# Performance work log

Hardware: AMD Instinct MI355X
Metric: run time of the kernel (lower is better)

Reference implementation:

```python
import jax, jax.numpy as jnp
import numpy as np

NUM_NEIGHBORS = 9  # init kwarg num_neighbors


def euclidean_dist(x, y):
    # Pairwise L2 distance, matching PatchcoreModel.euclidean_dist
    x_norm = jnp.sum(x * x, axis=-1, keepdims=True)
    y_norm = jnp.sum(y * y, axis=-1, keepdims=True)
    res = x_norm - 2.0 * jnp.matmul(x, jnp.swapaxes(y, -2, -1)) + jnp.swapaxes(y_norm, -2, -1)
    return jnp.sqrt(jnp.maximum(res, 0.0))


def setup_inputs() -> dict:
    key = jax.random.key(0)
    k1, k2 = jax.random.split(key)
    B, W, H, D, M = 8, 28, 28, 384, 32768
    embedding = jax.random.normal(k1, (B * W * H, D), dtype=jnp.float32)
    memory_bank = jax.random.normal(k2, (M, D), dtype=jnp.float32)
    return {"embedding": embedding, "memory_bank": memory_bank,
            "batch_size": B, "width": W, "height": H}


def reference(embedding, memory_bank, batch_size, width, height):
    # nearest_neighbors(embedding, n_neighbors=1)
    d = euclidean_dist(embedding, memory_bank)          # [N, M]
    patch_scores = jnp.min(d, axis=1)                   # [N]
    locations = jnp.argmin(d, axis=1)                   # [N]

    ps = patch_scores.reshape(batch_size, -1)           # [B, P]
    loc = locations.reshape(batch_size, -1)             # [B, P]

    # compute_anomaly_score (num_neighbors > 1 path)
    bidx = jnp.arange(batch_size)
    max_patches = jnp.argmax(ps, axis=1)                # [B]
    emb_b = embedding.reshape(batch_size, -1, embedding.shape[-1])
    max_feats = emb_b[bidx, max_patches]                # [B, D]
    score = ps[bidx, max_patches]                       # [B]
    nn_index = loc[bidx, max_patches]                   # [B]
    nn_sample = memory_bank[nn_index]                   # [B, D]

    k = min(NUM_NEIGHBORS, memory_bank.shape[0])
    d2 = euclidean_dist(nn_sample, memory_bank)         # [B, M]
    _, support = jax.lax.top_k(-d2, k)                  # k smallest, ascending

    d3 = euclidean_dist(max_feats[:, None, :], memory_bank[support])  # [B, 1, k]
    weights = (1.0 - jax.nn.softmax(d3[:, 0, :], axis=1))[:, 0]       # [B]
    pred_score = weights * score                        # [B]

    patch_map = ps.reshape(batch_size, 1, width, height)
    return patch_map, pred_score
```

## Files before the change

kernel.cpp:

```cpp
#include <hip/hip_runtime.h>
#include <hip/hip_bf16.h>

#define NROWS 6272
#define MROWS 32768
#define DDIM  384
#define NB    8
#define PPB   784
#define BN    128
#define BMT   128
#define MSPLIT 16
#define MC    (MROWS / MSPLIT)
#define MTILES (MC / BMT)
#define NSTEPS (MTILES * 12)
#define PSW   (MSPLIT * 2)
#define KNN   9
#define TSEG  16
#define TOPT  3
#define NRESC (NB * TOPT)

typedef float f32x4 __attribute__((ext_vector_type(4)));
typedef short bf16x8 __attribute__((ext_vector_type(8)));

__device__ __forceinline__ unsigned short f2bf(float f) {
  union { float f; unsigned int u; } c; c.f = f;
  unsigned int u = c.u + 0x7FFFu + ((c.u >> 16) & 1u);
  return (unsigned short)(u >> 16);
}
__device__ __forceinline__ unsigned int pk2(float a, float b) {
  return (unsigned int)f2bf(a) | ((unsigned int)f2bf(b) << 16);
}
__device__ __forceinline__ float wredsum(float v) {
#pragma unroll
  for (int m = 32; m; m >>= 1) v += __shfl_xor(v, m, 64);
  return v;
}
__device__ __forceinline__ void glds16(const void* g, void* l) {
  __builtin_amdgcn_global_load_lds(
      (const __attribute__((address_space(1))) unsigned int*)g,
      (__attribute__((address_space(3))) unsigned int*)l, 16, 0, 0);
}

__global__ __launch_bounds__(256) void cvt_bf16_kernel(
    const float* __restrict__ src, unsigned short* __restrict__ dst) {
  const int i = blockIdx.x * 256 + threadIdx.x;
  const float4 a = ((const float4*)src)[i * 2];
  const float4 b = ((const float4*)src)[i * 2 + 1];
  uint4 o = { pk2(a.x, a.y), pk2(a.z, a.w), pk2(b.x, b.y), pk2(b.z, b.w) };
  ((uint4*)dst)[i] = o;
}

__global__ __launch_bounds__(256) void rownorm_kernel(
    const float* __restrict__ src, float* __restrict__ nrm) {
  const int wave = threadIdx.x >> 6, lane = threadIdx.x & 63;
  const int m = blockIdx.x * 4 + wave;
  const float* y = src + (size_t)m * DDIM;
  float s = 0.f;
#pragma unroll
  for (int j = 0; j < 6; ++j) { float v = y[lane + 64 * j]; s = fmaf(v, v, s); }
  s = wredsum(s);
  if (lane == 0) nrm[m] = s;
}

__global__ __launch_bounds__(256) void dist_min_kernel(
    const unsigned short* __restrict__ embbf, const unsigned short* __restrict__ bankbf,
    const float* __restrict__ ynorm, float* __restrict__ psPart) {
  __shared__ unsigned short Al[2][4096];
  __shared__ unsigned short Bl[2][4096];
  __shared__ float ynLds[MC];

  const int bid = blockIdx.x;
  const int ms = bid & (MSPLIT - 1);
  const int bn = bid >> 4;
  const int t = threadIdx.x;
  const int lane = t & 63;
  const int wave = t >> 6;
  const int wn = wave >> 1, wm = wave & 1;
  const int l15 = lane & 15, l4 = lane >> 4;

  for (int i = t; i < MC; i += 256) ynLds[i] = ynorm[ms * MC + i];

  const int seg0 = wave * 2, seg1 = seg0 + 1;
  const int sRow = lane >> 2;
  const int sColB = (lane & 3) * 16;
  const char* aG0 = (const char*)embbf + ((size_t)(bn * BN + seg0 * 16 + sRow)) * 768 + sColB;
  const char* aG1 = (const char*)embbf + ((size_t)(bn * BN + seg1 * 16 + sRow)) * 768 + sColB;
  const char* bG0 = (const char*)bankbf + ((size_t)(ms * MC + seg0 * 16 + sRow)) * 768 + sColB;
  const char* bG1 = (const char*)bankbf + ((size_t)(ms * MC + seg1 * 16 + sRow)) * 768 + sColB;

  auto stage = [&](int st, int buf) {
    const int kb = (st % 12) * 64;
    const size_t bOff = (size_t)(st / 12) * (BMT * 768);
    glds16(aG0 + kb, &Al[buf][seg0 * 512]);
    glds16(aG1 + kb, &Al[buf][seg1 * 512]);
    glds16(bG0 + bOff + kb, &Bl[buf][seg0 * 512]);
    glds16(bG1 + bOff + kb, &Bl[buf][seg1 * 512]);
  };

  f32x4 acc[4][4];
#pragma unroll
  for (int nf = 0; nf < 4; ++nf)
#pragma unroll
    for (int mf = 0; mf < 4; ++mf) {
      acc[nf][mf][0] = 0.f; acc[nf][mf][1] = 0.f;
      acc[nf][mf][2] = 0.f; acc[nf][mf][3] = 0.f;
    }
  float rm[4][4];
#pragma unroll
  for (int a = 0; a < 4; ++a)
#pragma unroll
    for (int b = 0; b < 4; ++b) rm[a][b] = 3.4e38f;

  stage(0, 0);
  __syncthreads();

  for (int st = 0; st < NSTEPS; ++st) {
    const int buf = st & 1;
    if (st < NSTEPS - 1) stage(st + 1, buf ^ 1);

    bf16x8 af[4], bfr[4];
#pragma unroll
    for (int nf = 0; nf < 4; ++nf)
      af[nf] = *(const bf16x8*)&Al[buf][(wn * 64 + nf * 16 + l15) * 32 + l4 * 8];
#pragma unroll
    for (int mf = 0; mf < 4; ++mf)
      bfr[mf] = *(const bf16x8*)&Bl[buf][(wm * 64 + mf * 16 + l15) * 32 + l4 * 8];
#pragma unroll
    for (int nf = 0; nf < 4; ++nf)
#pragma unroll
      for (int mf = 0; mf < 4; ++mf)
        acc[nf][mf] = __builtin_amdgcn_mfma_f32_16x16x32_bf16(
            af[nf], bfr[mf], acc[nf][mf], 0, 0, 0);

    if ((st % 12) == 11) {
      const int mt = st / 12;
      const int mb = mt * BMT + wm * 64 + l15;
#pragma unroll
      for (int mf = 0; mf < 4; ++mf) {
        const float yv = ynLds[mb + mf * 16];
#pragma unroll
        for (int nf = 0; nf < 4; ++nf)
#pragma unroll
          for (int r = 0; r < 4; ++r)
            rm[nf][r] = fminf(rm[nf][r], fmaf(-2.f, acc[nf][mf][r], yv));
      }
#pragma unroll
      for (int nf = 0; nf < 4; ++nf)
#pragma unroll
        for (int mf = 0; mf < 4; ++mf) {
          acc[nf][mf][0] = 0.f; acc[nf][mf][1] = 0.f;
          acc[nf][mf][2] = 0.f; acc[nf][mf][3] = 0.f;
        }
    }
    __syncthreads();
  }

#pragma unroll
  for (int nf = 0; nf < 4; ++nf)
#pragma unroll
    for (int r = 0; r < 4; ++r) {
      float v = rm[nf][r];
      v = fminf(v, __shfl_xor(v, 1, 64));
      v = fminf(v, __shfl_xor(v, 2, 64));
      v = fminf(v, __shfl_xor(v, 4, 64));
      v = fminf(v, __shfl_xor(v, 8, 64));
      if (l15 == 0) {
        const int n = bn * BN + wn * 64 + nf * 16 + l4 * 4 + r;
        psPart[(size_t)n * PSW + ms * 2 + wm] = v;
      }
    }
}

__global__ __launch_bounds__(256) void ps_reduce_kernel(
    const float* __restrict__ psPart, const float* __restrict__ xnorm,
    float* __restrict__ out) {
  const int n = blockIdx.x * 256 + threadIdx.x;
  if (n >= NROWS) return;
  const float4* p = (const float4*)(psPart + (size_t)n * PSW);
  float m = 3.4e38f;
#pragma unroll
  for (int j = 0; j < 8; ++j) {
    const float4 a = p[j];
    m = fminf(m, fminf(fminf(a.x, a.y), fminf(a.z, a.w)));
  }
  out[n] = sqrtf(fmaxf(xnorm[n] + m, 0.f));
}

__global__ __launch_bounds__(256) void argmax3_kernel(
    const float* __restrict__ ps, int* __restrict__ trow) {
  __shared__ float vals[PPB];
  __shared__ float sv[256]; __shared__ int si[256];
  const int b = blockIdx.x, t = threadIdx.x;
  for (int p = t; p < PPB; p += 256) vals[p] = ps[b * PPB + p];
  __syncthreads();
  for (int k = 0; k < TOPT; ++k) {
    float best = -3.4e38f; int bi = 0x7FFFFFFF;
    for (int p = t; p < PPB; p += 256) {
      const float v = vals[p];
      if (v > best || (v == best && p < bi)) { best = v; bi = p; }
    }
    sv[t] = best; si[t] = bi;
    __syncthreads();
    for (int s = 128; s > 0; s >>= 1) {
      if (t < s) {
        if (sv[t + s] > sv[t] || (sv[t + s] == sv[t] && si[t + s] < si[t])) {
          sv[t] = sv[t + s]; si[t] = si[t + s];
        }
      }
      __syncthreads();
    }
    if (t == 0) { trow[b * TOPT + k] = b * PPB + si[0]; vals[si[0]] = -3.4e38f; }
    __syncthreads();
  }
}

__global__ __launch_bounds__(256) void rescue_kernel(
    const float* __restrict__ emb, const float* __restrict__ bank,
    const float* __restrict__ ynorm, const int* __restrict__ trow,
    float* __restrict__ rscV, int* __restrict__ rscI) {
  __shared__ float xs[NRESC][DDIM];
  __shared__ int sTrow[NRESC];
  __shared__ float pvw[4][NRESC]; __shared__ int piw[4][NRESC];
  const int t = threadIdx.x, lane = t & 63, wave = t >> 6;
  if (t < NRESC) sTrow[t] = trow[t];
  __syncthreads();
  for (int j = 0; j < NRESC; ++j)
    for (int k = t; k < DDIM; k += 256) xs[j][k] = emb[(size_t)sTrow[j] * DDIM + k];
  __syncthreads();

  const int m = blockIdx.x * 256 + t;
  const float yn = ynorm[m];
  const float* y = bank + (size_t)m * DDIM;
  float accs[NRESC];
#pragma unroll
  for (int j = 0; j < NRESC; ++j) accs[j] = yn;
  for (int k = 0; k < DDIM; ++k) {
    const float bk2 = -2.f * y[k];
#pragma unroll
    for (int j = 0; j < NRESC; ++j) accs[j] = fmaf(bk2, xs[j][k], accs[j]);
  }
#pragma unroll
  for (int j = 0; j < NRESC; ++j) {
    float v = accs[j]; int mi = m;
#pragma unroll
    for (int s = 1; s < 64; s <<= 1) {
      const float ov = __shfl_xor(v, s, 64);
      const int oi = __shfl_xor(mi, s, 64);
      if (ov < v || (ov == v && oi < mi)) { v = ov; mi = oi; }
    }
    if (lane == 0) { pvw[wave][j] = v; piw[wave][j] = mi; }
  }
  __syncthreads();
  if (t < NRESC) {
    float bv = pvw[0][t]; int bi = piw[0][t];
#pragma unroll
    for (int w = 1; w < 4; ++w)
      if (pvw[w][t] < bv || (pvw[w][t] == bv && piw[w][t] < bi)) { bv = pvw[w][t]; bi = piw[w][t]; }
    rscV[(size_t)t * 128 + blockIdx.x] = bv;
    rscI[(size_t)t * 128 + blockIdx.x] = bi;
  }
}

__global__ __launch_bounds__(256) void rescue_merge_kernel(
    const float* __restrict__ emb, const int* __restrict__ trow,
    const float* __restrict__ rscV, const int* __restrict__ rscI,
    float* __restrict__ score, int* __restrict__ maxrow, int* __restrict__ nnidx) {
  __shared__ float xnLds[NRESC];
  __shared__ float exv[NRESC]; __shared__ int exi[NRESC];
  const int t = threadIdx.x, lane = t & 63, wave = t >> 6;
  for (int q = 0; q < 6; ++q) {
    const int j = wave * 6 + q;
    const float* x = emb + (size_t)trow[j] * DDIM;
    float s = 0.f;
#pragma unroll
    for (int e = 0; e < 6; ++e) { const float v = x[lane + 64 * e]; s = fmaf(v, v, s); }
    s = wredsum(s);
    if (lane == 0) xnLds[j] = s;
  }
  __syncthreads();
  if (t < NRESC) {
    float bv = 3.4e38f; int bi = 0x7FFFFFFF;
    for (int i = 0; i < 128; ++i) {
      const float v = rscV[(size_t)t * 128 + i];
      if (v < bv) { bv = v; bi = rscI[(size_t)t * 128 + i]; }
      else if (v == bv) { const int oi = rscI[(size_t)t * 128 + i]; if (oi < bi) bi = oi; }
    }
    exv[t] = sqrtf(fmaxf(xnLds[t] + bv, 0.f));
    exi[t] = bi;
  }
  __syncthreads();
  if (t < NB) {
    float best = -3.4e38f; int bj = 0, brow = 0x7FFFFFFF;
    for (int k = 0; k < TOPT; ++k) {
      const int j = t * TOPT + k;
      const int row = trow[j];
      if (exv[j] > best || (exv[j] == best && row < brow)) { best = exv[j]; bj = j; brow = row; }
    }
    score[t] = best; maxrow[t] = brow; nnidx[t] = exi[bj];
  }
}

__global__ __launch_bounds__(256) void d2_kernel(
    const float* __restrict__ bank, const float* __restrict__ ynorm,
    const int* __restrict__ nnidx, float* __restrict__ d2) {
  __shared__ float nnf[NB][DDIM];
  __shared__ float nno[NB];
  const int t = threadIdx.x;
  for (int b = 0; b < NB; ++b) {
    const int m = nnidx[b];
    for (int j = t; j < DDIM; j += 256) nnf[b][j] = bank[(size_t)m * DDIM + j];
  }
  if (t < NB) nno[t] = ynorm[nnidx[t]];
  __syncthreads();
  const int wave = t >> 6, lane = t & 63;
  const int m = blockIdx.x * 4 + wave;
  const float* y = bank + (size_t)m * DDIM;
  float yv[6];
#pragma unroll
  for (int j = 0; j < 6; ++j) yv[j] = y[lane + 64 * j];
  const float yn = ynorm[m];
  for (int b = 0; b < NB; ++b) {
    float d = 0.f;
#pragma unroll
    for (int j = 0; j < 6; ++j) d = fmaf(yv[j], nnf[b][lane + 64 * j], d);
    d = wredsum(d);
    if (lane == 0) d2[(size_t)b * MROWS + m] = fmaxf(fmaf(-2.f, d, nno[b] + yn), 0.f);
  }
}

__global__ __launch_bounds__(256) void topk1_kernel(
    const float* __restrict__ d2, float* __restrict__ tv, int* __restrict__ ti) {
  __shared__ float sv[256]; __shared__ int si[256];
  const int b = blockIdx.x / TSEG, seg = blockIdx.x % TSEG;
  const float* base = d2 + (size_t)b * MROWS + seg * 2048;
  const int t = threadIdx.x, off = t * 8;
  float v[8];
  const float4 x0 = *(const float4*)(base + off);
  const float4 x1 = *(const float4*)(base + off + 4);
  v[0] = x0.x; v[1] = x0.y; v[2] = x0.z; v[3] = x0.w;
  v[4] = x1.x; v[5] = x1.y; v[6] = x1.z; v[7] = x1.w;
  for (int k = 0; k < KNN; ++k) {
    float lb = v[0]; int li = 0;
#pragma unroll
    for (int i = 1; i < 8; ++i)
      if (v[i] < lb) { lb = v[i]; li = i; }
    sv[t] = lb; si[t] = off + li;
    __syncthreads();
    for (int s = 128; s > 0; s >>= 1) {
      if (t < s) {
        if (sv[t + s] < sv[t] || (sv[t + s] == sv[t] && si[t + s] < si[t])) {
          sv[t] = sv[t + s]; si[t] = si[t + s];
        }
      }
      __syncthreads();
    }
    const int widx = si[0];
    if (t == 0) {
      tv[(size_t)(b * TSEG + seg) * KNN + k] = sv[0];
      ti[(size_t)(b * TSEG + seg) * KNN + k] = seg * 2048 + widx;
    }
    __syncthreads();
#pragma unroll
    for (int i = 0; i < 8; ++i)
      if (off + i == widx) v[i] = 3.4e38f;
  }
}

__global__ __launch_bounds__(64) void topk2_kernel(
    const float* __restrict__ tv, const int* __restrict__ ti, int* __restrict__ support) {
  const int b = blockIdx.x, lane = threadIdx.x;
  float v[3]; int ix[3];
#pragma unroll
  for (int j = 0; j < 3; ++j) {
    const int e = lane + j * 64;
    if (e < TSEG * KNN) { v[j] = tv[(size_t)b * TSEG * KNN + e]; ix[j] = ti[(size_t)b * TSEG * KNN + e]; }
    else { v[j] = 3.4e38f; ix[j] = 0x7FFFFFFF; }
  }
  for (int k = 0; k < KNN; ++k) {
    float bv = v[0]; int bi = ix[0];
#pragma unroll
    for (int j = 1; j < 3; ++j)
      if (v[j] < bv || (v[j] == bv && ix[j] < bi)) { bv = v[j]; bi = ix[j]; }
#pragma unroll
    for (int m = 1; m < 64; m <<= 1) {
      const float ov = __shfl_xor(bv, m, 64);
      const int oi = __shfl_xor(bi, m, 64);
      if (ov < bv || (ov == bv && oi < bi)) { bv = ov; bi = oi; }
    }
    if (lane == 0) support[b * KNN + k] = bi;
#pragma unroll
    for (int j = 0; j < 3; ++j)
      if (ix[j] == bi) v[j] = 3.4e38f;
  }
}

__global__ __launch_bounds__(256) void final_kernel(
    const float* __restrict__ emb, const float* __restrict__ bank,
    const float* __restrict__ ynorm, const int* __restrict__ support,
    const int* __restrict__ maxrow, const float* __restrict__ score,
    float* __restrict__ pred) {
  __shared__ float d3s[NB][KNN];
  const int t = threadIdx.x, wave = t >> 6, lane = t & 63;
  for (int b = wave; b < NB; b += 4) {
    const float* x = emb + (size_t)maxrow[b] * DDIM;
    float xv[6];
#pragma unroll
    for (int j = 0; j < 6; ++j) xv[j] = x[lane + 64 * j];
    float xn = 0.f;
#pragma unroll
    for (int j = 0; j < 6; ++j) xn = fmaf(xv[j], xv[j], xn);
    xn = wredsum(xn);
    for (int k = 0; k < KNN; ++k) {
      const int m = support[b * KNN + k];
      const float* y = bank + (size_t)m * DDIM;
      float d = 0.f;
#pragma unroll
      for (int j = 0; j < 6; ++j) d = fmaf(xv[j], y[lane + 64 * j], d);
      d = wredsum(d);
      if (lane == 0) d3s[b][k] = sqrtf(fmaxf(fmaf(-2.f, d, xn + ynorm[m]), 0.f));
    }
  }
  __syncthreads();
  if (t < NB) {
    float mx = -3.4e38f;
    for (int k = 0; k < KNN; ++k) mx = fmaxf(mx, d3s[t][k]);
    float sum = 0.f, e0 = 0.f;
    for (int k = 0; k < KNN; ++k) {
      const float e = expf(d3s[t][k] - mx);
      if (k == 0) e0 = e;
      sum += e;
    }
    pred[t] = (1.f - e0 / sum) * score[t];
  }
}

extern "C" void kernel_launch(void* const* d_in, const int* in_sizes, int n_in,
                              void* d_out, int out_size, void* d_ws, size_t ws_size,
                              hipStream_t stream) {
  (void)in_sizes; (void)n_in; (void)out_size; (void)ws_size;
  const float* emb = (const float*)d_in[0];
  const float* bank = (const float*)d_in[1];
  float* out = (float*)d_out;

  char* ws = (char*)d_ws;
  size_t o = 0;
  auto alloc = [&](size_t bytes) { void* p = ws + o; o = (o + bytes + 255) & ~(size_t)255; return p; };
  float* ynorm = (float*)alloc((size_t)MROWS * 4);
  float* xnorm = (float*)alloc((size_t)NROWS * 4);
  unsigned short* embbf = (unsigned short*)alloc((size_t)NROWS * DDIM * 2);
  unsigned short* bankbf = (unsigned short*)alloc((size_t)MROWS * DDIM * 2);
  float* psPart = (float*)alloc((size_t)NROWS * PSW * 4);
  int* trow = (int*)alloc(NRESC * 4);
  float* rscV = (float*)alloc((size_t)NRESC * 128 * 4);
  int* rscI = (int*)alloc((size_t)NRESC * 128 * 4);
  float* d2 = (float*)alloc((size_t)NB * MROWS * 4);
  float* tv = (float*)alloc((size_t)NB * TSEG * KNN * 4);
  int* ti = (int*)alloc((size_t)NB * TSEG * KNN * 4);
  float* score = (float*)alloc(256);
  int* maxrow = (int*)alloc(256);
  int* nnidx = (int*)alloc(256);
  int* support = (int*)alloc(512);

  cvt_bf16_kernel<<<NROWS * DDIM / 8 / 256, 256, 0, stream>>>(emb, embbf);
  cvt_bf16_kernel<<<MROWS * DDIM / 8 / 256, 256, 0, stream>>>(bank, bankbf);
  rownorm_kernel<<<MROWS / 4, 256, 0, stream>>>(bank, ynorm);
  rownorm_kernel<<<NROWS / 4, 256, 0, stream>>>(emb, xnorm);
  dist_min_kernel<<<(NROWS / BN) * MSPLIT, 256, 0, stream>>>(embbf, bankbf, ynorm, psPart);
  ps_reduce_kernel<<<(NROWS + 255) / 256, 256, 0, stream>>>(psPart, xnorm, out);
  argmax3_kernel<<<NB, 256, 0, stream>>>(out, trow);
  rescue_kernel<<<MROWS / 256, 256, 0, stream>>>(emb, bank, ynorm, trow, rscV, rscI);
  rescue_merge_kernel<<<1, 256, 0, stream>>>(emb, trow, rscV, rscI, score, maxrow, nnidx);
  d2_kernel<<<MROWS / 4, 256, 0, stream>>>(bank, ynorm, nnidx, d2);
  topk1_kernel<<<NB * TSEG, 256, 0, stream>>>(d2, tv, ti);
  topk2_kernel<<<NB, 64, 0, stream>>>(tv, ti, support);
  final_kernel<<<1, 256, 0, stream>>>(emb, bank, ynorm, support, maxrow, score, out + NROWS);
}
```

Baseline: 624.4 us.

## Swizzle LDS tiles, double M split, and restructure rescue kernel per-wave

```diff
diff --git a/kernel.cpp b/kernel.cpp
--- a/kernel.cpp
+++ b/kernel.cpp
@@ -8,15 +8,16 @@
 #define PPB   784
 #define BN    128
 #define BMT   128
-#define MSPLIT 16
+#define MSPLIT 32
 #define MC    (MROWS / MSPLIT)
 #define MTILES (MC / BMT)
 #define NSTEPS (MTILES * 12)
 #define PSW   (MSPLIT * 2)
 #define KNN   9
 #define TSEG  16
-#define TOPT  3
+#define TOPT  4
 #define NRESC (NB * TOPT)
+#define NPART 2048
 
 typedef float f32x4 __attribute__((ext_vector_type(4)));
 typedef short bf16x8 __attribute__((ext_vector_type(8)));
@@ -66,22 +67,20 @@
     const float* __restrict__ ynorm, float* __restrict__ psPart) {
   __shared__ unsigned short Al[2][4096];
   __shared__ unsigned short Bl[2][4096];
-  __shared__ float ynLds[MC];
 
   const int bid = blockIdx.x;
   const int ms = bid & (MSPLIT - 1);
-  const int bn = bid >> 4;
+  const int bn = bid >> 5;
   const int t = threadIdx.x;
   const int lane = t & 63;
   const int wave = t >> 6;
   const int wn = wave >> 1, wm = wave & 1;
   const int l15 = lane & 15, l4 = lane >> 4;
 
-  for (int i = t; i < MC; i += 256) ynLds[i] = ynorm[ms * MC + i];
-
   const int seg0 = wave * 2, seg1 = seg0 + 1;
   const int sRow = lane >> 2;
-  const int sColB = (lane & 3) * 16;
+  const int srcSlot = (lane & 3) ^ ((sRow >> 1) & 3);
+  const int sColB = srcSlot * 16;
   const char* aG0 = (const char*)embbf + ((size_t)(bn * BN + seg0 * 16 + sRow)) * 768 + sColB;
   const char* aG1 = (const char*)embbf + ((size_t)(bn * BN + seg1 * 16 + sRow)) * 768 + sColB;
   const char* bG0 = (const char*)bankbf + ((size_t)(ms * MC + seg0 * 16 + sRow)) * 768 + sColB;
@@ -96,6 +95,8 @@
     glds16(bG1 + bOff + kb, &Bl[buf][seg1 * 512]);
   };
 
+  const int rdSlot = (l4 ^ ((l15 >> 1) & 3)) * 8;
+
   f32x4 acc[4][4];
 #pragma unroll
   for (int nf = 0; nf < 4; ++nf)
@@ -110,6 +111,8 @@
 #pragma unroll
     for (int b = 0; b < 4; ++b) rm[a][b] = 3.4e38f;
 
+  const float* ynG = ynorm + ms * MC;
+
   stage(0, 0);
   __syncthreads();
 
@@ -120,10 +123,10 @@
     bf16x8 af[4], bfr[4];
 #pragma unroll
     for (int nf = 0; nf < 4; ++nf)
-      af[nf] = *(const bf16x8*)&Al[buf][(wn * 64 + nf * 16 + l15) * 32 + l4 * 8];
+      af[nf] = *(const bf16x8*)&Al[buf][(wn * 64 + nf * 16 + l15) * 32 + rdSlot];
 #pragma unroll
     for (int mf = 0; mf < 4; ++mf)
-      bfr[mf] = *(const bf16x8*)&Bl[buf][(wm * 64 + mf * 16 + l15) * 32 + l4 * 8];
+      bfr[mf] = *(const bf16x8*)&Bl[buf][(wm * 64 + mf * 16 + l15) * 32 + rdSlot];
 #pragma unroll
     for (int nf = 0; nf < 4; ++nf)
 #pragma unroll
@@ -136,7 +139,7 @@
       const int mb = mt * BMT + wm * 64 + l15;
 #pragma unroll
       for (int mf = 0; mf < 4; ++mf) {
-        const float yv = ynLds[mb + mf * 16];
+        const float yv = ynG[mb + mf * 16];
 #pragma unroll
         for (int nf = 0; nf < 4; ++nf)
 #pragma unroll
@@ -178,14 +181,14 @@
   const float4* p = (const float4*)(psPart + (size_t)n * PSW);
   float m = 3.4e38f;
 #pragma unroll
-  for (int j = 0; j < 8; ++j) {
+  for (int j = 0; j < PSW / 4; ++j) {
     const float4 a = p[j];
     m = fminf(m, fminf(fminf(a.x, a.y), fminf(a.z, a.w)));
   }
   out[n] = sqrtf(fmaxf(xnorm[n] + m, 0.f));
 }
 
-__global__ __launch_bounds__(256) void argmax3_kernel(
+__global__ __launch_bounds__(256) void argmax4_kernel(
     const float* __restrict__ ps, int* __restrict__ trow) {
   __shared__ float vals[PPB];
   __shared__ float sv[256]; __shared__ int si[256];
@@ -217,37 +220,44 @@
     const float* __restrict__ emb, const float* __restrict__ bank,
     const float* __restrict__ ynorm, const int* __restrict__ trow,
     float* __restrict__ rscV, int* __restrict__ rscI) {
-  __shared__ float xs[NRESC][DDIM];
+  __shared__ float xs[NRESC * DDIM];
   __shared__ int sTrow[NRESC];
   __shared__ float pvw[4][NRESC]; __shared__ int piw[4][NRESC];
   const int t = threadIdx.x, lane = t & 63, wave = t >> 6;
   if (t < NRESC) sTrow[t] = trow[t];
   __syncthreads();
-  for (int j = 0; j < NRESC; ++j)
-    for (int k = t; k < DDIM; k += 256) xs[j][k] = emb[(size_t)sTrow[j] * DDIM + k];
-  __syncthreads();
-
-  const int m = blockIdx.x * 256 + t;
-  const float yn = ynorm[m];
-  const float* y = bank + (size_t)m * DDIM;
-  float accs[NRESC];
-#pragma unroll
-  for (int j = 0; j < NRESC; ++j) accs[j] = yn;
-  for (int k = 0; k < DDIM; ++k) {
-    const float bk2 = -2.f * y[k];
-#pragma unroll
-    for (int j = 0; j < NRESC; ++j) accs[j] = fmaf(bk2, xs[j][k], accs[j]);
-  }
-#pragma unroll
+  for (int idx = t; idx < NRESC * (DDIM / 4); idx += 256) {
+    const int j = idx / (DDIM / 4), c = idx % (DDIM / 4);
+    ((float4*)xs)[idx] = ((const float4*)(emb + (size_t)sTrow[j] * DDIM))[c];
+  }
+  __syncthreads();
+
+  const int m0 = blockIdx.x * 16 + wave * 4;
+  float yv[4][6]; float yn[4];
+#pragma unroll
+  for (int q = 0; q < 4; ++q) {
+    const float* y = bank + (size_t)(m0 + q) * DDIM;
+#pragma unroll
+    for (int e = 0; e < 6; ++e) yv[q][e] = y[lane + 64 * e];
+    yn[q] = ynorm[m0 + q];
+  }
+
   for (int j = 0; j < NRESC; ++j) {
-    float v = accs[j]; int mi = m;
-#pragma unroll
-    for (int s = 1; s < 64; s <<= 1) {
-      const float ov = __shfl_xor(v, s, 64);
-      const int oi = __shfl_xor(mi, s, 64);
-      if (ov < v || (ov == v && oi < mi)) { v = ov; mi = oi; }
-    }
-    if (lane == 0) { pvw[wave][j] = v; piw[wave][j] = mi; }
+    float s0 = 0.f, s1 = 0.f, s2 = 0.f, s3 = 0.f;
+#pragma unroll
+    for (int e = 0; e < 6; ++e) {
+      const float xe = xs[j * DDIM + lane + 64 * e];
+      s0 = fmaf(yv[0][e], xe, s0);
+      s1 = fmaf(yv[1][e], xe, s1);
+      s2 = fmaf(yv[2][e], xe, s2);
+      s3 = fmaf(yv[3][e], xe, s3);
+    }
+    s0 = wredsum(s0); s1 = wredsum(s1); s2 = wredsum(s2); s3 = wredsum(s3);
+    float bv = fmaf(-2.f, s0, yn[0]); int bi = m0;
+    float v1 = fmaf(-2.f, s1, yn[1]); if (v1 < bv) { bv = v1; bi = m0 + 1; }
+    float v2 = fmaf(-2.f, s2, yn[2]); if (v2 < bv) { bv = v2; bi = m0 + 2; }
+    float v3 = fmaf(-2.f, s3, yn[3]); if (v3 < bv) { bv = v3; bi = m0 + 3; }
+    if (lane == 0) { pvw[wave][j] = bv; piw[wave][j] = bi; }
   }
   __syncthreads();
   if (t < NRESC) {
@@ -255,8 +265,8 @@
 #pragma unroll
     for (int w = 1; w < 4; ++w)
       if (pvw[w][t] < bv || (pvw[w][t] == bv && piw[w][t] < bi)) { bv = pvw[w][t]; bi = piw[w][t]; }
-    rscV[(size_t)t * 128 + blockIdx.x] = bv;
-    rscI[(size_t)t * 128 + blockIdx.x] = bi;
+    rscV[(size_t)t * NPART + blockIdx.x] = bv;
+    rscI[(size_t)t * NPART + blockIdx.x] = bi;
   }
 }
 
@@ -264,11 +274,22 @@
     const float* __restrict__ emb, const int* __restrict__ trow,
     const float* __restrict__ rscV, const int* __restrict__ rscI,
     float* __restrict__ score, int* __restrict__ maxrow, int* __restrict__ nnidx) {
+  __shared__ float mv[NRESC][8]; __shared__ int mi[NRESC][8];
   __shared__ float xnLds[NRESC];
   __shared__ float exv[NRESC]; __shared__ int exi[NRESC];
   const int t = threadIdx.x, lane = t & 63, wave = t >> 6;
-  for (int q = 0; q < 6; ++q) {
-    const int j = wave * 6 + q;
+  {
+    const int j = t >> 3, sl = t & 7;
+    float bv = 3.4e38f; int bi = 0x7FFFFFFF;
+    for (int i = sl * (NPART / 8); i < (sl + 1) * (NPART / 8); ++i) {
+      const float v = rscV[(size_t)j * NPART + i];
+      if (v < bv) { bv = v; bi = rscI[(size_t)j * NPART + i]; }
+      else if (v == bv) { const int oi = rscI[(size_t)j * NPART + i]; if (oi < bi) bi = oi; }
+    }
+    mv[j][sl] = bv; mi[j][sl] = bi;
+  }
+  for (int q = 0; q < 8; ++q) {
+    const int j = wave * 8 + q;
     const float* x = emb + (size_t)trow[j] * DDIM;
     float s = 0.f;
 #pragma unroll
@@ -278,12 +299,10 @@
   }
   __syncthreads();
   if (t < NRESC) {
-    float bv = 3.4e38f; int bi = 0x7FFFFFFF;
-    for (int i = 0; i < 128; ++i) {
-      const float v = rscV[(size_t)t * 128 + i];
-      if (v < bv) { bv = v; bi = rscI[(size_t)t * 128 + i]; }
-      else if (v == bv) { const int oi = rscI[(size_t)t * 128 + i]; if (oi < bi) bi = oi; }
-    }
+    float bv = mv[t][0]; int bi = mi[t][0];
+#pragma unroll
+    for (int s = 1; s < 8; ++s)
+      if (mv[t][s] < bv || (mv[t][s] == bv && mi[t][s] < bi)) { bv = mv[t][s]; bi = mi[t][s]; }
     exv[t] = sqrtf(fmaxf(xnLds[t] + bv, 0.f));
     exi[t] = bi;
   }
@@ -450,8 +469,8 @@
   unsigned short* bankbf = (unsigned short*)alloc((size_t)MROWS * DDIM * 2);
   float* psPart = (float*)alloc((size_t)NROWS * PSW * 4);
   int* trow = (int*)alloc(NRESC * 4);
-  float* rscV = (float*)alloc((size_t)NRESC * 128 * 4);
-  int* rscI = (int*)alloc((size_t)NRESC * 128 * 4);
+  float* rscV = (float*)alloc((size_t)NRESC * NPART * 4);
+  int* rscI = (int*)alloc((size_t)NRESC * NPART * 4);
   float* d2 = (float*)alloc((size_t)NB * MROWS * 4);
   float* tv = (float*)alloc((size_t)NB * TSEG * KNN * 4);
   int* ti = (int*)alloc((size_t)NB * TSEG * KNN * 4);
@@ -466,8 +485,8 @@
   rownorm_kernel<<<NROWS / 4, 256, 0, stream>>>(emb, xnorm);
   dist_min_kernel<<<(NROWS / BN) * MSPLIT, 256, 0, stream>>>(embbf, bankbf, ynorm, psPart);
   ps_reduce_kernel<<<(NROWS + 255) / 256, 256, 0, stream>>>(psPart, xnorm, out);
-  argmax3_kernel<<<NB, 256, 0, stream>>>(out, trow);
-  rescue_kernel<<<MROWS / 256, 256, 0, stream>>>(emb, bank, ynorm, trow, rscV, rscI);
+  argmax4_kernel<<<NB, 256, 0, stream>>>(out, trow);
+  rescue_kernel<<<NPART, 256, 0, stream>>>(emb, bank, ynorm, trow, rscV, rscI);
   rescue_merge_kernel<<<1, 256, 0, stream>>>(emb, trow, rscV, rscI, score, maxrow, nnidx);
   d2_kernel<<<MROWS / 4, 256, 0, stream>>>(bank, ynorm, nnidx, d2);
   topk1_kernel<<<NB * TSEG, 256, 0, stream>>>(d2, tv, ti);
```

New measurement: 566.7 us. 1.1x faster.
